# Kernel optimization log

Hardware: AMD Instinct MI355X
Metric: run time of the kernel (lower is better)

## Reference

```python
import jax, jax.numpy as jnp
import numpy as np

B, T, C, H = 4, 2048, 1024, 16
HS = C // H  # head_size = 64


def setup_inputs() -> dict:
    key = jax.random.key(0)
    ks = jax.random.split(key, 6)
    s = C ** -0.5  # Linear default init scale (approx, kaiming-uniform-ish)
    x = jax.random.normal(ks[0], (B, T, C), dtype=jnp.float32)
    Wq = jax.random.normal(ks[1], (H, C, HS), dtype=jnp.float32) * s
    Wk = jax.random.normal(ks[2], (H, C, HS), dtype=jnp.float32) * s
    Wv = jax.random.normal(ks[3], (H, C, HS), dtype=jnp.float32) * s
    Wproj = jax.random.normal(ks[4], (C, C), dtype=jnp.float32) * s
    bproj = jax.random.normal(ks[5], (C,), dtype=jnp.float32) * s
    return {"x": x, "Wq": Wq, "Wk": Wk, "Wv": Wv, "Wproj": Wproj, "bproj": bproj}


def reference(x, Wq, Wk, Wv, Wproj, bproj):
    # Batched multi-head attention equivalent to looping over per-head modules.
    # q,k,v: (B, H, T, HS)
    q = jnp.einsum('btc,hcd->bhtd', x, Wq)
    k = jnp.einsum('btc,hcd->bhtd', x, Wk)
    v = jnp.einsum('btc,hcd->bhtd', x, Wv)
    scale = HS ** -0.5
    scores = jnp.einsum('bhqd,bhkd->bhqk', q, k) * scale  # (B,H,T,T)
    causal = jnp.tril(jnp.ones((T, T), dtype=bool))
    scores = jnp.where(causal, scores, -jnp.inf)
    wei = jax.nn.softmax(scores, axis=-1)
    out_heads = jnp.einsum('bhqk,bhkd->bhqd', wei, v)  # (B,H,T,HS)
    # concat heads along last dim -> (B,T,H*HS) = (B,T,C)
    combo = out_heads.transpose(0, 2, 1, 3).reshape(B, T, C)
    out = jnp.einsum('btc,cd->btd', combo, Wproj.T.T @ jnp.eye(C, dtype=combo.dtype)) if False else combo @ Wproj.T + bproj
    # dropout p=0.0 (eval) -> identity
    return out
```

## Files before the change

### kernel.cpp

```cpp
#include <hip/hip_runtime.h>
#include <stdint.h>

#define B_  4
#define T_  2048
#define C_  1024
#define H_  16
#define HS_ 64
#define M_  (B_*T_)
#define K_  C_

typedef unsigned short u16;
typedef float v4f __attribute__((ext_vector_type(4)));
typedef short v8s __attribute__((ext_vector_type(8)));
typedef u16   v4u __attribute__((ext_vector_type(4)));
typedef unsigned int u32;
typedef u32 v2u32 __attribute__((ext_vector_type(2)));

__device__ __forceinline__ u16 f2bf(float f){
  unsigned u = __float_as_uint(f);
  u += 0x7fffu + ((u >> 16) & 1u);
  return (u16)(u >> 16);
}

__device__ __forceinline__ u32 cvt_pk_bf16(float a, float b){
  u32 r;
  asm("v_cvt_pk_bf16_f32 %0, %1, %2" : "=v"(r) : "v"(a), "v"(b));
  return r;
}

__device__ __forceinline__ void async16(const void* g, void* l){
  __builtin_amdgcn_global_load_lds(
      (const __attribute__((address_space(1))) unsigned int*)g,
      (__attribute__((address_space(3))) unsigned int*)l,
      16, 0, 0);
}


__global__ __launch_bounds__(256)
void prep(const float* __restrict__ x,
          const float* __restrict__ Wq, const float* __restrict__ Wk,
          const float* __restrict__ Wv, const float* __restrict__ Wproj,
          u16* __restrict__ xhat, u16* __restrict__ wallT, u16* __restrict__ wprojT)
{
  const int bid = blockIdx.x;
  if (bid < 4096){
    int gid = bid * 256 + threadIdx.x;
    int r  = gid >> 7;
    int kg = gid & 127;
    const float* s = x + ((size_t)r << 10) + (kg << 3);
    v4f a = *(const v4f*)s;
    v4f b = *(const v4f*)(s + 4);
    union { v8s v; u16 e[8]; } o;
    o.e[0]=f2bf(a[0]); o.e[1]=f2bf(a[1]); o.e[2]=f2bf(a[2]); o.e[3]=f2bf(a[3]);
    o.e[4]=f2bf(b[0]); o.e[5]=f2bf(b[1]); o.e[6]=f2bf(b[2]); o.e[7]=f2bf(b[3]);
    *(v8s*)(xhat + (((size_t)(r >> 4) * 128 + kg) * 128 + ((r & 15) << 3))) = o.v;
  } else if (bid < 5632){
    int gid = (bid - 4096) * 256 + threadIdx.x;
    int n  = gid >> 7;
    int cg = gid & 127;
    int tensor = n >> 10;
    int h = (n >> 6) & 15;
    int d = n & 63;
    const float* W = (tensor == 0) ? Wq : ((tensor == 1) ? Wk : Wv);
    const float* base = W + ((size_t)(h * C_ + cg * 8)) * HS_ + d;
    union { v8s v; u16 e[8]; } o;
    #pragma unroll
    for (int j = 0; j < 8; j++) o.e[j] = f2bf(base[(size_t)j * HS_]);
    *(v8s*)(wallT + (((size_t)(n >> 4) * 128 + cg) * 128 + ((n & 15) << 3))) = o.v;
  } else {
    int gid = (bid - 5632) * 256 + threadIdx.x;
    int r  = gid >> 7;
    int kg = gid & 127;
    const float* s = Wproj + ((size_t)r << 10) + (kg << 3);
    v4f a = *(const v4f*)s;
    v4f b = *(const v4f*)(s + 4);
    union { v8s v; u16 e[8]; } o;
    o.e[0]=f2bf(a[0]); o.e[1]=f2bf(a[1]); o.e[2]=f2bf(a[2]); o.e[3]=f2bf(a[3]);
    o.e[4]=f2bf(b[0]); o.e[5]=f2bf(b[1]); o.e[6]=f2bf(b[2]); o.e[7]=f2bf(b[3]);
    *(v8s*)(wprojT + (((size_t)(r >> 4) * 128 + kg) * 128 + ((r & 15) << 3))) = o.v;
  }
}

#define QSCALE 0.1803368801111204f

template<int MODE>
__global__ __launch_bounds__(256)
void gemm_bt(const u16* __restrict__ A, const u16* __restrict__ Bt,
             const float* __restrict__ bias,
             u16* __restrict__ o0, u16* __restrict__ o1, u16* __restrict__ o2,
             float* __restrict__ o0f)
{
  __shared__ __align__(16) u16 sA[2][128 * 32];
  __shared__ __align__(16) u16 sB[2][128 * 32];
  const int tid  = threadIdx.x;
  const int lane = tid & 63;
  const int wave = tid >> 6;
  const int l15  = lane & 15, quad = lane >> 4;
  const int wm   = wave >> 1, wn = wave & 1;
  const int m0   = blockIdx.y * 128;
  const int n0   = blockIdx.x * 128;
  const int mg0  = blockIdx.y * 8;
  const int ng0  = blockIdx.x * 8;

  v4f acc[4][4] = {};

  const int s0 = tid, s1 = tid + 256;
  const int t0 = s0 >> 6, r0 = s0 & 15, g0 = (s0 >> 4) & 3;
  const int t1 = s1 >> 6, r1 = s1 & 15, g1 = (s1 >> 4) & 3;

  const char* aS0 = (const char*)A  + ((size_t)(mg0 + t0) * 16384 + g0 * 128 + r0 * 8) * 2;
  const char* aS1 = (const char*)A  + ((size_t)(mg0 + t1) * 16384 + g1 * 128 + r1 * 8) * 2;
  const char* bS0 = (const char*)Bt + ((size_t)(ng0 + t0) * 16384 + g0 * 128 + r0 * 8) * 2;
  const char* bS1 = (const char*)Bt + ((size_t)(ng0 + t1) * 16384 + g1 * 128 + r1 * 8) * 2;

  async16(aS0, (char*)sA[0] + s0 * 16);
  async16(aS1, (char*)sA[0] + s1 * 16);
  async16(bS0, (char*)sB[0] + s0 * 16);
  async16(bS1, (char*)sB[0] + s1 * 16);
  __syncthreads();

  int cur = 0;
  for (int kk = 0; kk < K_; kk += 32){
    const int nxt = cur ^ 1;
    if (kk + 32 < K_){
      const size_t off = (size_t)(kk + 32) * 32;
      async16(aS0 + off, (char*)sA[nxt] + s0 * 16);
      async16(aS1 + off, (char*)sA[nxt] + s1 * 16);
      async16(bS0 + off, (char*)sB[nxt] + s0 * 16);
      async16(bS1 + off, (char*)sB[nxt] + s1 * 16);
    }

    v8s af[4], bfr[4];
    const u16* pa = sA[cur] + (size_t)(wm * 4) * 512 + lane * 8;
    const u16* pb = sB[cur] + (size_t)(wn * 4) * 512 + lane * 8;
    #pragma unroll
    for (int mi = 0; mi < 4; mi++) af[mi]  = *(const v8s*)(pa + mi * 512);
    #pragma unroll
    for (int ni = 0; ni < 4; ni++) bfr[ni] = *(const v8s*)(pb + ni * 512);

    #pragma unroll
    for (int mi = 0; mi < 4; mi++)
      #pragma unroll
      for (int ni = 0; ni < 4; ni++)
        acc[mi][ni] = __builtin_amdgcn_mfma_f32_16x16x32_bf16(af[mi], bfr[ni], acc[mi][ni], 0, 0, 0);

    __syncthreads();
    cur = nxt;
  }

  if constexpr (MODE == 0){
    #pragma unroll
    for (int ni = 0; ni < 4; ni++){
      const int ng = n0 + wn * 64 + ni * 16 + l15;
      const int tensor = ng >> 10;
      const int hh = (ng >> 6) & 15;
      const int d  = ng & 63;
      #pragma unroll
      for (int mi = 0; mi < 4; mi++){
        const int mbase = m0 + wm * 64 + mi * 16 + quad * 4;
        const int bb = mbase >> 11;
        const int tt = mbase & 2047;
        if (tensor == 2){
          v4u pk;
          #pragma unroll
          for (int r = 0; r < 4; r++) pk[r] = f2bf(acc[mi][ni][r]);
          *(v4u*)(o2 + ((size_t)((bb * H_ + hh) * HS_ + d)) * T_ + tt) = pk;
        } else if (tensor == 0){
          #pragma unroll
          for (int r = 0; r < 4; r++)
            o0[((size_t)((bb * H_ + hh)) * T_ + tt + r) * HS_ + d] = f2bf(acc[mi][ni][r] * QSCALE);
        } else {
          #pragma unroll
          for (int r = 0; r < 4; r++)
            o1[((size_t)((bb * H_ + hh)) * T_ + tt + r) * HS_ + d] = f2bf(acc[mi][ni][r]);
        }
      }
    }
  } else {
    #pragma unroll
    for (int ni = 0; ni < 4; ni++){
      const int ng = n0 + wn * 64 + ni * 16 + l15;
      const float bv = bias[ng];
      #pragma unroll
      for (int mi = 0; mi < 4; mi++){
        const int mbase = m0 + wm * 64 + mi * 16 + quad * 4;
        #pragma unroll
        for (int r = 0; r < 4; r++)
          o0f[(size_t)(mbase + r) * C_ + ng] = acc[mi][ni][r] + bv;
      }
    }
  }
}

__global__ __launch_bounds__(512, 4)
void attn(const u16* __restrict__ Q, const u16* __restrict__ Kb_, const u16* __restrict__ Vt,
          u16* __restrict__ O)
{
  __shared__ __align__(16) u16 sK[64 * 64];
  __shared__ __align__(16) u16 sV[64 * 64];
  __shared__ __align__(16) u16 Plds[8][16][88];
  const int tid  = threadIdx.x;
  const int lane = tid & 63;
  const int wave = tid >> 6;
  const int l15  = lane & 15, quad = lane >> 4;
  const int pp   = blockIdx.y & 7;
  const int bh   = blockIdx.x * 8 + (blockIdx.y >> 3);

  const u16* Qb = Q   + (size_t)bh * T_ * HS_;
  const u16* Kb = Kb_ + (size_t)bh * T_ * HS_;
  const u16* Vb = Vt  + (size_t)bh * HS_ * T_;
  const int b = bh >> 4, h = bh & 15;

  const int g  = tid;
  const int tg = g >> 3;
  const int sw = ((g & 7) ^ (tg & 7)) << 4;
  const char* Kby = (const char*)Kb;
  const char* Vby = (const char*)Vb;
  const int koff = tg * 128 + sw;
  const int voff = tg * (T_ * 2) + sw;
  char* sKp = (char*)sK + g * 16;
  char* sVp = (char*)sV + g * 16;

  const int fsw0 = (quad ^ (l15 & 7)) * 8;
  const int fsw1 = ((quad + 4) ^ (l15 & 7)) * 8;

  #pragma unroll 1
  for (int ph = 0; ph < 2; ph++){
    const int qt = ph ? (15 - pp) : pp;
    const int q0 = qt * 128 + wave * 16;

    const v8s qf0 = *(const v8s*)(Qb + (size_t)(q0 + l15) * HS_ + quad * 8);
    const v8s qf1 = *(const v8s*)(Qb + (size_t)(q0 + l15) * HS_ + 32 + quad * 8);

    v4f Oa[4] = {};
    float lsum = 0.f;

    const int ktmax = 2 * qt + 1;
    for (int kt = 0; kt <= ktmax; kt++){
      const int k0 = kt * 64;
      async16(Kby + (size_t)k0 * 128 + koff, sKp);
      async16(Vby + (size_t)k0 * 2   + voff, sVp);
      __syncthreads();

      if (k0 <= q0 + 15){
        v4f sacc[4] = {};
        __builtin_amdgcn_s_setprio(1);
        #pragma unroll
        for (int nt = 0; nt < 4; nt++){
          const u16* kr = sK + (nt * 16 + l15) * 64;
          v8s kf0 = *(const v8s*)(kr + fsw0);
          v8s kf1 = *(const v8s*)(kr + fsw1);
          sacc[nt] = __builtin_amdgcn_mfma_f32_16x16x32_bf16(kf0, qf0, sacc[nt], 0, 0, 0);
          sacc[nt] = __builtin_amdgcn_mfma_f32_16x16x32_bf16(kf1, qf1, sacc[nt], 0, 0, 0);
        }
        __builtin_amdgcn_s_setprio(0);
        const bool diag = (k0 + 63 > q0);
        const int qrow_rel = (q0 - k0) + l15;

        #pragma unroll
        for (int nt = 0; nt < 4; nt++){
          float p0 = exp2f(sacc[nt][0]);
          float p1 = exp2f(sacc[nt][1]);
          float p2 = exp2f(sacc[nt][2]);
          float p3 = exp2f(sacc[nt][3]);
          if (diag){
            const int kbase = nt * 16 + quad * 4;
            if (kbase + 0 > qrow_rel) p0 = 0.f;
            if (kbase + 1 > qrow_rel) p1 = 0.f;
            if (kbase + 2 > qrow_rel) p2 = 0.f;
            if (kbase + 3 > qrow_rel) p3 = 0.f;
          }
          lsum += (p0 + p1) + (p2 + p3);
          v2u32 w;
          w[0] = cvt_pk_bf16(p0, p1);
          w[1] = cvt_pk_bf16(p2, p3);
          *(v2u32*)&Plds[wave][l15][nt * 16 + quad * 4] = w;
        }

        asm volatile("" ::: "memory");
        const v8s pf0 = *(const v8s*)&Plds[wave][l15][quad * 8];
        const v8s pf1 = *(const v8s*)&Plds[wave][l15][32 + quad * 8];
        __builtin_amdgcn_s_setprio(1);
        #pragma unroll
        for (int nt = 0; nt < 4; nt++){
          const u16* vr = sV + (nt * 16 + l15) * 64;
          v8s vf0 = *(const v8s*)(vr + fsw0);
          v8s vf1 = *(const v8s*)(vr + fsw1);
          Oa[nt] = __builtin_amdgcn_mfma_f32_16x16x32_bf16(pf0, vf0, Oa[nt], 0, 0, 0);
          Oa[nt] = __builtin_amdgcn_mfma_f32_16x16x32_bf16(pf1, vf1, Oa[nt], 0, 0, 0);
        }
        __builtin_amdgcn_s_setprio(0);
      }
      __syncthreads();
    }

    float rs = lsum;
    rs += __shfl_xor(rs, 16);
    rs += __shfl_xor(rs, 32);
    const int mg = b * 128 + qt * 8 + wave;
    #pragma unroll
    for (int reg = 0; reg < 4; reg++){
      const float rsq = __shfl(rs, quad * 4 + reg);
      const float inv = (rsq > 0.f) ? (1.f / rsq) : 0.f;
      const int mrow = quad * 4 + reg;
      #pragma unroll
      for (int nt = 0; nt < 4; nt++){
        const int cg = h * 8 + nt * 2 + (l15 >> 3);
        O[((size_t)mg * 128 + cg) * 128 + mrow * 8 + (l15 & 7)] = f2bf(Oa[nt][reg] * inv);
      }
    }
  }
}

extern "C" void kernel_launch(void* const* d_in, const int* in_sizes, int n_in,
                              void* d_out, int out_size, void* d_ws, size_t ws_size,
                              hipStream_t stream)
{
  const float* x     = (const float*)d_in[0];
  const float* Wq    = (const float*)d_in[1];
  const float* Wk    = (const float*)d_in[2];
  const float* Wv    = (const float*)d_in[3];
  const float* Wproj = (const float*)d_in[4];
  const float* bproj = (const float*)d_in[5];
  float* out = (float*)d_out;

  u16* xhat   = (u16*)d_ws;
  u16* att    = xhat;
  u16* q_ws   = xhat  + (size_t)M_ * C_;
  u16* k_ws   = q_ws  + (size_t)M_ * C_;
  u16* vt_ws  = k_ws  + (size_t)M_ * C_;
  u16* wallT  = vt_ws + (size_t)M_ * C_;
  u16* wprojT = wallT + (size_t)3 * C_ * K_;

  prep<<<dim3(6144), dim3(256), 0, stream>>>(x, Wq, Wk, Wv, Wproj, xhat, wallT, wprojT);
  gemm_bt<0><<<dim3(24, 64), dim3(256), 0, stream>>>(xhat, wallT, nullptr,
                                                     q_ws, k_ws, vt_ws, nullptr);
  attn<<<dim3(8, 64), dim3(512), 0, stream>>>(q_ws, k_ws, vt_ws, att);
  gemm_bt<1><<<dim3(8, 64), dim3(256), 0, stream>>>(att, wprojT, bproj,
                                                    nullptr, nullptr, nullptr, out);
}
```

Measured before the change: 281.3 us.

## Enlarge GEMM block tile to 256x128 with 512-thread blocks

Both projection GEMMs now use 8 waves per block computing a 256x128 output tile, instead of 4 waves computing 128x128. The grid is halved along M, and the async global-to-LDS load mapping is rewritten to fill the taller A tile. Each B tile is shared across twice as many rows, which is meant to cut global and L2 traffic for the weight operand. In exchange, each block uses more LDS, the grid has fewer blocks, and the launch bound caps registers at a level that may squeeze the 64-float accumulator.

New measurement: 282.0 us. Within noise of the previous version (+0.3%).

```diff
diff --git a/kernel.cpp b/kernel.cpp
--- a/kernel.cpp
+++ b/kernel.cpp
@@ -84,50 +84,47 @@
 #define QSCALE 0.1803368801111204f
 
 template<int MODE>
-__global__ __launch_bounds__(256)
+__global__ __launch_bounds__(512, 4)
 void gemm_bt(const u16* __restrict__ A, const u16* __restrict__ Bt,
              const float* __restrict__ bias,
              u16* __restrict__ o0, u16* __restrict__ o1, u16* __restrict__ o2,
              float* __restrict__ o0f)
 {
-  __shared__ __align__(16) u16 sA[2][128 * 32];
-  __shared__ __align__(16) u16 sB[2][128 * 32];
+  __shared__ __align__(16) u16 sA[2][16 * 512];
+  __shared__ __align__(16) u16 sB[2][8 * 512];
   const int tid  = threadIdx.x;
   const int lane = tid & 63;
   const int wave = tid >> 6;
   const int l15  = lane & 15, quad = lane >> 4;
-  const int wm   = wave >> 1, wn = wave & 1;
-  const int m0   = blockIdx.y * 128;
+  const int wm   = wave >> 1;
+  const int wn   = wave & 1;
+  const int m0   = blockIdx.y * 256;
   const int n0   = blockIdx.x * 128;
-  const int mg0  = blockIdx.y * 8;
+  const int mg0  = blockIdx.y * 16;
   const int ng0  = blockIdx.x * 8;
 
   v4f acc[4][4] = {};
 
-  const int s0 = tid, s1 = tid + 256;
-  const int t0 = s0 >> 6, r0 = s0 & 15, g0 = (s0 >> 4) & 3;
-  const int t1 = s1 >> 6, r1 = s1 & 15, g1 = (s1 >> 4) & 3;
-
-  const char* aS0 = (const char*)A  + ((size_t)(mg0 + t0) * 16384 + g0 * 128 + r0 * 8) * 2;
-  const char* aS1 = (const char*)A  + ((size_t)(mg0 + t1) * 16384 + g1 * 128 + r1 * 8) * 2;
-  const char* bS0 = (const char*)Bt + ((size_t)(ng0 + t0) * 16384 + g0 * 128 + r0 * 8) * 2;
-  const char* bS1 = (const char*)Bt + ((size_t)(ng0 + t1) * 16384 + g1 * 128 + r1 * 8) * 2;
-
-  async16(aS0, (char*)sA[0] + s0 * 16);
-  async16(aS1, (char*)sA[0] + s1 * 16);
-  async16(bS0, (char*)sB[0] + s0 * 16);
-  async16(bS1, (char*)sB[0] + s1 * 16);
+  const int sa0 = tid, sa1 = tid + 512;
+  const char* Ab = (const char*)A;
+  const char* Bb = (const char*)Bt;
+  const char* aG0 = Ab + (size_t)(mg0 + (sa0 >> 6)) * 32768 + (size_t)(sa0 & 63) * 16;
+  const char* aG1 = Ab + (size_t)(mg0 + (sa1 >> 6)) * 32768 + (size_t)(sa1 & 63) * 16;
+  const char* bG0 = Bb + (size_t)(ng0 + (tid >> 6)) * 32768 + (size_t)(tid & 63) * 16;
+
+  async16(aG0, (char*)sA[0] + sa0 * 16);
+  async16(aG1, (char*)sA[0] + sa1 * 16);
+  async16(bG0, (char*)sB[0] + tid * 16);
   __syncthreads();
 
   int cur = 0;
-  for (int kk = 0; kk < K_; kk += 32){
+  for (int t = 0; t < K_ / 32; ++t){
     const int nxt = cur ^ 1;
-    if (kk + 32 < K_){
-      const size_t off = (size_t)(kk + 32) * 32;
-      async16(aS0 + off, (char*)sA[nxt] + s0 * 16);
-      async16(aS1 + off, (char*)sA[nxt] + s1 * 16);
-      async16(bS0 + off, (char*)sB[nxt] + s0 * 16);
-      async16(bS1 + off, (char*)sB[nxt] + s1 * 16);
+    if (t + 1 < K_ / 32){
+      const size_t off = (size_t)(t + 1) * 1024;
+      async16(aG0 + off, (char*)sA[nxt] + sa0 * 16);
+      async16(aG1 + off, (char*)sA[nxt] + sa1 * 16);
+      async16(bG0 + off, (char*)sB[nxt] + tid * 16);
     }
 
     v8s af[4], bfr[4];
@@ -333,9 +330,9 @@
   u16* wprojT = wallT + (size_t)3 * C_ * K_;
 
   prep<<<dim3(6144), dim3(256), 0, stream>>>(x, Wq, Wk, Wv, Wproj, xhat, wallT, wprojT);
-  gemm_bt<0><<<dim3(24, 64), dim3(256), 0, stream>>>(xhat, wallT, nullptr,
+  gemm_bt<0><<<dim3(24, 32), dim3(512), 0, stream>>>(xhat, wallT, nullptr,
                                                      q_ws, k_ws, vt_ws, nullptr);
   attn<<<dim3(8, 64), dim3(512), 0, stream>>>(q_ws, k_ws, vt_ws, att);
-  gemm_bt<1><<<dim3(8, 64), dim3(256), 0, stream>>>(att, wprojT, bproj,
+  gemm_bt<1><<<dim3(8, 32), dim3(512), 0, stream>>>(att, wprojT, bproj,
                                                     nullptr, nullptr, nullptr, out);
 }
```
